# Performance work log

Hardware: AMD Instinct MI355X
Metric: run time of the kernel (lower is better)

Reference implementation:

```python
import jax, jax.numpy as jnp
import numpy as np

N_NODES = 100000
N_EDGES = 3200000
N_GRAPHS = 2000
F_IN, H, N_CLS = 14, 64, 2


def _glorot(key, shape):
    lim = float(np.sqrt(6.0 / (shape[0] + shape[1])))
    return jax.random.uniform(key, shape, jnp.float32, -lim, lim)


def setup_inputs() -> dict:
    key = jax.random.key(0)
    ks = jax.random.split(key, 16)
    x = jax.random.normal(ks[0], (N_NODES, F_IN), jnp.float32)
    edge_index = jax.random.randint(ks[1], (2, N_EDGES), 0, N_NODES, jnp.int64)
    batch = jnp.sort(jax.random.randint(ks[2], (N_NODES,), 0, N_GRAPHS, jnp.int64))
    return {
        "x": x,
        "W1l": _glorot(ks[3], (F_IN, H)), "W1r": _glorot(ks[4], (F_IN, H)), "b1": jnp.zeros((H,), jnp.float32),
        "W2l": _glorot(ks[5], (H, H)), "W2r": _glorot(ks[6], (H, H)), "b2": jnp.zeros((H,), jnp.float32),
        "W3l": _glorot(ks[7], (H, H)), "W3r": _glorot(ks[8], (H, H)), "b3": jnp.zeros((H,), jnp.float32),
        "W4l": _glorot(ks[9], (H, N_CLS)), "W4r": _glorot(ks[10], (H, N_CLS)), "b4": jnp.zeros((N_CLS,), jnp.float32),
        "edge_index": edge_index,
        "batch": batch,
    }


def _sage_conv(x, Wl, Wr, b, src, dst, inv_deg):
    # mean-aggregate neighbor features: messages flow src -> dst (PyG SAGEConv default)
    agg = jax.ops.segment_sum(x[src], dst, num_segments=N_NODES) * inv_deg
    return agg @ Wl + x @ Wr + b


def reference(x, W1l, W1r, b1, W2l, W2r, b2, W3l, W3r, b3, W4l, W4r, b4, edge_index, batch):
    src, dst = edge_index[0], edge_index[1]
    ones = jnp.ones((src.shape[0],), x.dtype)
    deg = jax.ops.segment_sum(ones, dst, num_segments=N_NODES)
    inv_deg = (1.0 / jnp.maximum(deg, 1.0))[:, None]  # [N,1], isolated nodes -> 0 agg

    h = jax.nn.relu(_sage_conv(x, W1l, W1r, b1, src, dst, inv_deg))
    h = jax.nn.relu(_sage_conv(h, W2l, W2r, b2, src, dst, inv_deg))
    h = jax.nn.relu(_sage_conv(h, W3l, W3r, b3, src, dst, inv_deg))
    h = _sage_conv(h, W4l, W4r, b4, src, dst, inv_deg)

    # global_mean_pool over graphs
    gsum = jax.ops.segment_sum(h, batch, num_segments=N_GRAPHS)
    gcnt = jax.ops.segment_sum(jnp.ones((h.shape[0],), h.dtype), batch, num_segments=N_GRAPHS)
    pooled = gsum / jnp.maximum(gcnt, 1.0)[:, None]
    return jax.nn.log_softmax(pooled, axis=-1)
```

## Files before the change

kernel.cpp:

```cpp
#include <hip/hip_runtime.h>

#define NN 100000
#define NE 3200000
#define NG 2000
#define FIN 14
#define HD 64
#define NC 2

#define NBUK 256
#define BNODES 391
#define P1E 4096
#define BUFCAP 13312

typedef unsigned int uint;

__device__ __forceinline__ uint pack2bf16(float a, float b) {
    uint ua = __float_as_uint(a), ub = __float_as_uint(b);
    ua = (ua + 0x7FFFu + ((ua >> 16) & 1u)) >> 16;
    ub = (ub + 0x7FFFu + ((ub >> 16) & 1u)) >> 16;
    return ua | (ub << 16);
}
__device__ __forceinline__ float bflo(uint u) { return __uint_as_float(u << 16); }
__device__ __forceinline__ float bfhi(uint u) { return __uint_as_float(u & 0xFFFF0000u); }


__global__ __launch_bounds__(256) void k_hist_bucket(const int* __restrict__ dst,
                                                     int* __restrict__ bkcnt) {
    __shared__ int cnt[NBUK];
    int t = threadIdx.x;
    cnt[t] = 0;
    __syncthreads();
    int e0 = blockIdx.x * P1E;
    int m = NE - e0; if (m > P1E) m = P1E;
    for (int e = t; e < m; e += 256) atomicAdd(&cnt[dst[e0 + e] / BNODES], 1);
    __syncthreads();
    if (cnt[t] > 0) atomicAdd(&bkcnt[t], cnt[t]);
}

__global__ void k_scanb(const int* __restrict__ bkcnt, int* __restrict__ bbase,
                        int* __restrict__ bcur) {
    __shared__ int tmp[NBUK];
    int t = threadIdx.x;
    int v = bkcnt[t];
    tmp[t] = v;
    __syncthreads();
    for (int off = 1; off < NBUK; off <<= 1) {
        int u = (t >= off) ? tmp[t - off] : 0;
        __syncthreads();
        tmp[t] += u;
        __syncthreads();
    }
    int excl = tmp[t] - v;
    bbase[t] = excl;
    bcur[t] = excl;
    if (t == NBUK - 1) bbase[NBUK] = tmp[t];
}

__global__ void k_gbounds(const int* __restrict__ batch, int* __restrict__ gstart,
                          int* __restrict__ gend) {
    int i = blockIdx.x * blockDim.x + threadIdx.x;
    if (i < NN) {
        int b = batch[i];
        if (i == 0 || batch[i - 1] != b) gstart[b] = i;
        if (i == NN - 1 || batch[i + 1] != b) gend[b] = i + 1;
    }
}

__global__ __launch_bounds__(256) void k_pass1(
    const int* __restrict__ src, const int* __restrict__ dst,
    int* __restrict__ bcur, int* __restrict__ pairs) {
    __shared__ int cnt[NBUK];
    __shared__ int scanb[NBUK + 1];
    __shared__ int cur[NBUK];
    __shared__ int gbase[NBUK];
    __shared__ int pbuf[P1E];
    __shared__ unsigned char bsl[P1E];
    int t = threadIdx.x;
    int e0 = blockIdx.x * P1E;
    int m = NE - e0; if (m > P1E) m = P1E;
    cnt[t] = 0;
    __syncthreads();
    int ds[16], ss[16], bk[16];
#pragma unroll
    for (int j = 0; j < 16; ++j) {
        int e = t + j * 256;
        if (e < m) {
            ds[j] = dst[e0 + e];
            ss[j] = src[e0 + e];
            bk[j] = ds[j] / BNODES;
            atomicAdd(&cnt[bk[j]], 1);
        } else bk[j] = -1;
    }
    __syncthreads();
    int v = cnt[t];
    scanb[t] = v;
    __syncthreads();
    for (int off = 1; off < 256; off <<= 1) {
        int u = (t >= off) ? scanb[t - off] : 0;
        __syncthreads();
        scanb[t] += u;
        __syncthreads();
    }
    int excl = scanb[t] - v;
    scanb[t] = excl;
    cur[t] = excl;
    if (t == 255) scanb[256] = excl + v;
    __syncthreads();
#pragma unroll
    for (int j = 0; j < 16; ++j) {
        if (bk[j] >= 0) {
            int p = atomicAdd(&cur[bk[j]], 1);
            pbuf[p] = ss[j] | ((ds[j] - bk[j] * BNODES) << 17);
            bsl[p] = (unsigned char)bk[j];
        }
    }
    int cb = scanb[t + 1] - scanb[t];
    if (cb > 0) gbase[t] = atomicAdd(&bcur[t], cb);
    __syncthreads();
    for (int s = t; s < m; s += 256) {
        int b = bsl[s];
        pairs[gbase[b] + (s - scanb[b])] = pbuf[s];
    }
}

__global__ __launch_bounds__(256) void k_pass2(
    const int* __restrict__ pairs, const int* __restrict__ bbase,
    int* __restrict__ deg, int* __restrict__ rs, int* __restrict__ csr) {
    __shared__ int buf1[BUFCAP];
    __shared__ int buf2[BUFCAP];
    __shared__ int cnt[512];
    __shared__ int rsl[512];
    __shared__ int cur[512];
    __shared__ int s1[256];
    int b = blockIdx.x;
    int n0 = b * BNODES;
    if (n0 >= NN) return;
    int nlocal = NN - n0; if (nlocal > BNODES) nlocal = BNODES;
    int t = threadIdx.x;
    int base = bbase[b];
    int m = bbase[b + 1] - base;
    bool fits = (m <= BUFCAP);
    cnt[t] = 0; cnt[t + 256] = 0;
    __syncthreads();
    for (int s = t; s < m; s += 256) {
        int pk = pairs[base + s];
        if (fits) buf1[s] = pk;
        atomicAdd(&cnt[(uint)pk >> 17], 1);
    }
    __syncthreads();
    int c0 = cnt[2 * t], c1 = cnt[2 * t + 1];
    int ps = c0 + c1;
    s1[t] = ps;
    __syncthreads();
    for (int off = 1; off < 256; off <<= 1) {
        int u = (t >= off) ? s1[t - off] : 0;
        __syncthreads();
        s1[t] += u;
        __syncthreads();
    }
    int pexcl = s1[t] - ps;
    rsl[2 * t] = pexcl;       cur[2 * t] = pexcl;
    rsl[2 * t + 1] = pexcl + c0; cur[2 * t + 1] = pexcl + c0;
    __syncthreads();
    for (int i = t; i < nlocal; i += 256) {
        deg[n0 + i] = cnt[i];
        rs[n0 + i] = base + rsl[i];
    }
    if (fits) {
        for (int s = t; s < m; s += 256) {
            int pk = buf1[s];
            int p = atomicAdd(&cur[(uint)pk >> 17], 1);
            buf2[p] = pk & 0x1FFFF;
        }
        __syncthreads();
        for (int s = t; s < m; s += 256) csr[base + s] = buf2[s];
    } else {
        for (int s = t; s < m; s += 256) {
            int pk = pairs[base + s];
            int p = atomicAdd(&cur[(uint)pk >> 17], 1);
            csr[base + p] = pk & 0x1FFFF;
        }
    }
}


__global__ void k_packx(const float* __restrict__ x, uint* __restrict__ xb) {
    int t = blockIdx.x * blockDim.x + threadIdx.x;
    if (t < NN * 8) {
        int row = t >> 3, q = t & 7;
        int j0 = 2 * q, j1 = 2 * q + 1;
        float f0 = (j0 < FIN) ? x[row * FIN + j0] : 0.f;
        float f1 = (j1 < FIN) ? x[row * FIN + j1] : 0.f;
        xb[t] = pack2bf16(f0, f1);
    }
}


__global__ __launch_bounds__(256, 6) void k_layer1(
    const float* __restrict__ x, const uint* __restrict__ xb, uint* __restrict__ hbout,
    const float* __restrict__ Wl, const float* __restrict__ Wr, const float* __restrict__ b,
    const int* __restrict__ rs, const int* __restrict__ deg, const int* __restrict__ csr) {
    __shared__ float2 sW[FIN][HD];
    __shared__ float sb[HD];
    __shared__ float2 sAH[4][16];
    for (int i = threadIdx.x; i < FIN * HD; i += 256) {
        int k = i >> 6, j = i & 63;
        sW[k][j] = make_float2(Wl[i], Wr[i]);
    }
    if (threadIdx.x < HD) sb[threadIdx.x] = b[threadIdx.x];
    __syncthreads();
    int lane = threadIdx.x & 63, wid = threadIdx.x >> 6;
    int sub = lane >> 3;
    int fq = lane & 7;
    int ngroups = (NN + 3) / 4;
    for (int g = blockIdx.x; g < ngroups; g += gridDim.x) {
        int n = g * 4 + wid;
        bool act = n < NN;
        if (act) {
            int s0 = rs[n], d = deg[n];
            float xv = (lane < FIN) ? x[n * FIN + lane] : 0.f;
            float2 a0 = make_float2(0.f, 0.f), a1 = a0, a2 = a0, a3 = a0;
            float2 a4 = a0, a5 = a0, a6 = a0, a7 = a0;
            for (int base = 0; base < d; base += 64) {
                int rem = d - base; if (rem > 64) rem = 64;
                int idxv = (lane < rem) ? csr[s0 + base + lane] : 0;
                int j = 0;
                for (; j + 64 <= rem; j += 64) {
                    int i0 = __shfl(idxv, j + 0 + sub);
                    int i1 = __shfl(idxv, j + 8 + sub);
                    int i2 = __shfl(idxv, j + 16 + sub);
                    int i3 = __shfl(idxv, j + 24 + sub);
                    int i4 = __shfl(idxv, j + 32 + sub);
                    int i5 = __shfl(idxv, j + 40 + sub);
                    int i6 = __shfl(idxv, j + 48 + sub);
                    int i7 = __shfl(idxv, j + 56 + sub);
                    uint u;
                    u = xb[(size_t)i0 * 8 + fq]; a0.x += bflo(u); a0.y += bfhi(u);
                    u = xb[(size_t)i1 * 8 + fq]; a1.x += bflo(u); a1.y += bfhi(u);
                    u = xb[(size_t)i2 * 8 + fq]; a2.x += bflo(u); a2.y += bfhi(u);
                    u = xb[(size_t)i3 * 8 + fq]; a3.x += bflo(u); a3.y += bfhi(u);
                    u = xb[(size_t)i4 * 8 + fq]; a4.x += bflo(u); a4.y += bfhi(u);
                    u = xb[(size_t)i5 * 8 + fq]; a5.x += bflo(u); a5.y += bfhi(u);
                    u = xb[(size_t)i6 * 8 + fq]; a6.x += bflo(u); a6.y += bfhi(u);
                    u = xb[(size_t)i7 * 8 + fq]; a7.x += bflo(u); a7.y += bfhi(u);
                }
                for (; j + 8 <= rem; j += 8) {
                    int i0 = __shfl(idxv, j + sub);
                    uint u = xb[(size_t)i0 * 8 + fq];
                    a0.x += bflo(u); a0.y += bfhi(u);
                }
                if (j < rem) {
                    int i0 = __shfl(idxv, j + sub);
                    if (sub < rem - j) {
                        uint u = xb[(size_t)i0 * 8 + fq];
                        a0.x += bflo(u); a0.y += bfhi(u);
                    }
                }
            }
            a0.x += a1.x + a2.x + a3.x + a4.x + a5.x + a6.x + a7.x;
            a0.y += a1.y + a2.y + a3.y + a4.y + a5.y + a6.y + a7.y;
            for (int off = 8; off <= 32; off <<= 1) {
                a0.x += __shfl_xor(a0.x, off);
                a0.y += __shfl_xor(a0.y, off);
            }
            float inv = 1.0f / (float)(d > 1 ? d : 1);
            float e0 = __shfl(a0.x, lane >> 1);
            float e1 = __shfl(a0.y, lane >> 1);
            float sel = (lane & 1) ? e1 : e0;
            if (lane < 16) sAH[wid][lane] = make_float2((lane < FIN) ? sel * inv : 0.f, xv);
        }
        float out = sb[lane];
#pragma unroll
        for (int k = 0; k < FIN; ++k) {
            float2 w = sW[k][lane];
            float2 ah = sAH[wid][k];
            out += ah.x * w.x + ah.y * w.y;
        }
        out = fmaxf(out, 0.f);
        float o2 = __shfl_xor(out, 1);
        if (act && !(lane & 1)) hbout[(size_t)n * 32 + (lane >> 1)] = pack2bf16(out, o2);
    }
}


__device__ __forceinline__ void bfadd4(float4& A, uint2 U) {
    A.x += bflo(U.x); A.y += bfhi(U.x);
    A.z += bflo(U.y); A.w += bfhi(U.y);
}

template <bool FUSEZ>
__global__ __launch_bounds__(256, 6) void k_layerH(
    const uint* __restrict__ hbin, uint* __restrict__ hbout,
    const float* __restrict__ Wl, const float* __restrict__ Wr, const float* __restrict__ b,
    const float* __restrict__ W4l, float* __restrict__ z,
    const int* __restrict__ rs, const int* __restrict__ deg, const int* __restrict__ csr) {
    __shared__ uint sWp[HD][HD];
    __shared__ float sb[HD], sW4l[HD * NC];
    __shared__ float2 sAH[4][HD];
    for (int i = threadIdx.x; i < HD * HD; i += 256) {
        int k = i >> 6, j = i & 63;
        sWp[k][j] = pack2bf16(Wl[i], Wr[i]);
    }
    if (threadIdx.x < HD) sb[threadIdx.x] = b[threadIdx.x];
    if (FUSEZ && threadIdx.x < HD * NC) sW4l[threadIdx.x] = W4l[threadIdx.x];
    __syncthreads();
    const uint2* hb2 = (const uint2*)hbin;
    int lane = threadIdx.x & 63, wid = threadIdx.x >> 6;
    int sub = lane >> 4;
    int fq = lane & 15;
    int ngroups = (NN + 3) / 4;
    for (int g = blockIdx.x; g < ngroups; g += gridDim.x) {
        int n = g * 4 + wid;
        bool act = n < NN;
        if (act) {
            int s0 = rs[n], d = deg[n];
            uint hu = hbin[(size_t)n * 32 + (lane >> 1)];
            float hv = (lane & 1) ? bfhi(hu) : bflo(hu);
            float4 A0 = make_float4(0.f, 0.f, 0.f, 0.f);
            float4 A1 = A0, A2 = A0, A3 = A0, A4 = A0, A5 = A0, A6 = A0, A7 = A0;
            for (int base = 0; base < d; base += 64) {
                int rem = d - base; if (rem > 64) rem = 64;
                int idxv = (lane < rem) ? csr[s0 + base + lane] : 0;
                int j = 0;
                for (; j + 32 <= rem; j += 32) {
                    int i0 = __shfl(idxv, j + 0 + sub);
                    int i1 = __shfl(idxv, j + 4 + sub);
                    int i2 = __shfl(idxv, j + 8 + sub);
                    int i3 = __shfl(idxv, j + 12 + sub);
                    int i4 = __shfl(idxv, j + 16 + sub);
                    int i5 = __shfl(idxv, j + 20 + sub);
                    int i6 = __shfl(idxv, j + 24 + sub);
                    int i7 = __shfl(idxv, j + 28 + sub);
                    bfadd4(A0, hb2[(size_t)i0 * 16 + fq]);
                    bfadd4(A1, hb2[(size_t)i1 * 16 + fq]);
                    bfadd4(A2, hb2[(size_t)i2 * 16 + fq]);
                    bfadd4(A3, hb2[(size_t)i3 * 16 + fq]);
                    bfadd4(A4, hb2[(size_t)i4 * 16 + fq]);
                    bfadd4(A5, hb2[(size_t)i5 * 16 + fq]);
                    bfadd4(A6, hb2[(size_t)i6 * 16 + fq]);
                    bfadd4(A7, hb2[(size_t)i7 * 16 + fq]);
                }
                for (; j + 4 <= rem; j += 4) {
                    int i0 = __shfl(idxv, j + sub);
                    bfadd4(A0, hb2[(size_t)i0 * 16 + fq]);
                }
                if (j < rem) {
                    int i0 = __shfl(idxv, j + sub);
                    if (sub < rem - j) bfadd4(A0, hb2[(size_t)i0 * 16 + fq]);
                }
            }
            A0.x += A1.x + A2.x + A3.x + A4.x + A5.x + A6.x + A7.x;
            A0.y += A1.y + A2.y + A3.y + A4.y + A5.y + A6.y + A7.y;
            A0.z += A1.z + A2.z + A3.z + A4.z + A5.z + A6.z + A7.z;
            A0.w += A1.w + A2.w + A3.w + A4.w + A5.w + A6.w + A7.w;
            for (int off = 16; off <= 32; off <<= 1) {
                A0.x += __shfl_xor(A0.x, off);
                A0.y += __shfl_xor(A0.y, off);
                A0.z += __shfl_xor(A0.z, off);
                A0.w += __shfl_xor(A0.w, off);
            }
            float inv = 1.0f / (float)(d > 1 ? d : 1);
            A0.x *= inv; A0.y *= inv; A0.z *= inv; A0.w *= inv;
            float e0 = __shfl(A0.x, lane >> 2);
            float e1 = __shfl(A0.y, lane >> 2);
            float e2 = __shfl(A0.z, lane >> 2);
            float e3 = __shfl(A0.w, lane >> 2);
            int c = lane & 3;
            float sel = (c == 0) ? e0 : (c == 1) ? e1 : (c == 2) ? e2 : e3;
            sAH[wid][lane] = make_float2(sel, hv);
        }
        float out = sb[lane];
#pragma unroll 8
        for (int k = 0; k < HD; ++k) {
            uint wu = sWp[k][lane];
            float2 ah = sAH[wid][k];
            out += ah.x * bflo(wu) + ah.y * bfhi(wu);
        }
        out = fmaxf(out, 0.f);
        float o2 = __shfl_xor(out, 1);
        if (act && !(lane & 1)) hbout[(size_t)n * 32 + (lane >> 1)] = pack2bf16(out, o2);
        if (FUSEZ) {
            float r0 = out * sW4l[lane * NC + 0];
            float r1 = out * sW4l[lane * NC + 1];
            for (int off = 32; off; off >>= 1) {
                r0 += __shfl_xor(r0, off);
                r1 += __shfl_xor(r1, off);
            }
            if (act && lane == 0) ((float2*)z)[n] = make_float2(r0, r1);
        }
    }
}


__global__ __launch_bounds__(256) void k_pool(
    const uint* __restrict__ h3, const float* __restrict__ z,
    const float* __restrict__ W4r, const float* __restrict__ b4,
    const int* __restrict__ rs, const int* __restrict__ deg, const int* __restrict__ csr,
    const int* __restrict__ batch, float* __restrict__ gsum) {
    __shared__ float sW[HD * NC];
    if (threadIdx.x < HD * NC) sW[threadIdx.x] = W4r[threadIdx.x];
    __syncthreads();
    const float2* z2 = (const float2*)z;
    int lane = threadIdx.x & 63, wid = threadIdx.x >> 6;
    int stride = gridDim.x * 4;
    for (int n = blockIdx.x * 4 + wid; n < NN; n += stride) {
        float r0 = 0.f, r1 = 0.f;
        if (lane < 32) {
            uint u = h3[(size_t)n * 32 + lane];
            float f0 = bflo(u), f1 = bfhi(u);
            r0 = f0 * sW[(2 * lane) * NC + 0] + f1 * sW[(2 * lane + 1) * NC + 0];
            r1 = f0 * sW[(2 * lane) * NC + 1] + f1 * sW[(2 * lane + 1) * NC + 1];
        }
        int s0 = rs[n], d = deg[n];
        float a0 = 0.f, a1 = 0.f;
        for (int j = lane; j < d; j += 64) {
            int s = csr[s0 + j];
            float2 zv = z2[s];
            a0 += zv.x;
            a1 += zv.y;
        }
        for (int off = 32; off; off >>= 1) {
            r0 += __shfl_xor(r0, off);
            r1 += __shfl_xor(r1, off);
            a0 += __shfl_xor(a0, off);
            a1 += __shfl_xor(a1, off);
        }
        if (lane == 0) {
            float inv = 1.0f / (float)(d > 1 ? d : 1);
            float o0 = a0 * inv + r0 + b4[0];
            float o1 = a1 * inv + r1 + b4[1];
            int gg = batch[n];
            atomicAdd(&gsum[gg * 2 + 0], o0);
            atomicAdd(&gsum[gg * 2 + 1], o1);
        }
    }
}

__global__ void k_final(const float* __restrict__ gsum, const int* __restrict__ gstart,
                        const int* __restrict__ gend, float* __restrict__ out) {
    int g = blockIdx.x * blockDim.x + threadIdx.x;
    if (g < NG) {
        int cnt = gend[g] - gstart[g];
        float inv = 1.0f / (float)(cnt > 1 ? cnt : 1);
        float p0 = gsum[g * 2 + 0] * inv;
        float p1 = gsum[g * 2 + 1] * inv;
        float m = fmaxf(p0, p1);
        float lse = m + logf(expf(p0 - m) + expf(p1 - m));
        out[g * 2 + 0] = p0 - lse;
        out[g * 2 + 1] = p1 - lse;
    }
}


extern "C" void kernel_launch(void* const* d_in, const int* in_sizes, int n_in,
                              void* d_out, int out_size, void* d_ws, size_t ws_size,
                              hipStream_t stream) {
    const float* x   = (const float*)d_in[0];
    const float* W1l = (const float*)d_in[1];
    const float* W1r = (const float*)d_in[2];
    const float* b1  = (const float*)d_in[3];
    const float* W2l = (const float*)d_in[4];
    const float* W2r = (const float*)d_in[5];
    const float* b2  = (const float*)d_in[6];
    const float* W3l = (const float*)d_in[7];
    const float* W3r = (const float*)d_in[8];
    const float* b3  = (const float*)d_in[9];
    const float* W4l = (const float*)d_in[10];
    const float* W4r = (const float*)d_in[11];
    const float* b4  = (const float*)d_in[12];
    const int* ei    = (const int*)d_in[13];
    const int* batch = (const int*)d_in[14];
    const int* src = ei;
    const int* dst = ei + NE;
    float* out = (float*)d_out;

    char* w = (char*)d_ws;
    int* deg    = (int*)w; w += (size_t)NN * 4;
    int* rs     = (int*)w; w += (size_t)NN * 4;
    int* csr    = (int*)w; w += (size_t)NE * 4;
    int* gstart = (int*)w; w += (size_t)NG * 4;
    int* gend   = (int*)w; w += (size_t)NG * 4;
    int* bkcnt  = (int*)w; w += NBUK * 4;
    int* bbase  = (int*)w; w += (NBUK + 1) * 4;
    int* bcur   = (int*)w; w += NBUK * 4;
    w = (char*)(((uintptr_t)w + 255) & ~(uintptr_t)255);
    uint* xb    = (uint*)w; w += (size_t)NN * 8 * 4;
    uint* hbA   = (uint*)w; w += (size_t)NN * 32 * 4;
    uint* hbB   = (uint*)w; w += (size_t)NN * 32 * 4;
    float* z    = (float*)w; w += (size_t)NN * NC * 4;
    float* gsum = (float*)w; w += (size_t)NG * NC * 4;
    int* pairs = (int*)hbB;

    const int P1B = (NE + P1E - 1) / P1E;

    hipMemsetAsync(bkcnt, 0, NBUK * 4, stream);
    hipMemsetAsync(gstart, 0, (size_t)NG * 4, stream);
    hipMemsetAsync(gend, 0, (size_t)NG * 4, stream);
    hipMemsetAsync(gsum, 0, (size_t)NG * NC * 4, stream);

    k_hist_bucket<<<P1B, 256, 0, stream>>>(dst, bkcnt);
    k_packx<<<(NN * 8 + 255) / 256, 256, 0, stream>>>(x, xb);
    k_gbounds<<<(NN + 255) / 256, 256, 0, stream>>>(batch, gstart, gend);
    k_scanb<<<1, NBUK, 0, stream>>>(bkcnt, bbase, bcur);
    k_pass1<<<P1B, 256, 0, stream>>>(src, dst, bcur, pairs);
    k_pass2<<<NBUK, 256, 0, stream>>>(pairs, bbase, deg, rs, csr);

    k_layer1<<<1536, 256, 0, stream>>>(x, xb, hbA, W1l, W1r, b1, rs, deg, csr);
    k_layerH<false><<<1536, 256, 0, stream>>>(hbA, hbB, W2l, W2r, b2, nullptr, nullptr, rs, deg, csr);
    k_layerH<true><<<1536, 256, 0, stream>>>(hbB, hbA, W3l, W3r, b3, W4l, z, rs, deg, csr);
    k_pool<<<2048, 256, 0, stream>>>(hbA, z, W4r, b4, rs, deg, csr, batch, gsum);
    k_final<<<(NG + 255) / 256, 256, 0, stream>>>(gsum, gstart, gend, out);
}
```

Before: 468.5 us.

## Tile hidden-layer gathers by source-node range so each pass stays cache-resident

The CSR build now sorts each destination's neighbors into eight source-node ranges and records per-range offsets in a new rs9 array. The hidden-layer kernels give each wave a fixed chunk of 25 destination nodes and sweep the source ranges in order. Per-node accumulators are kept in registers across sweeps, so that gathered feature rows come from a smaller, cache-resident slice of the feature table. In exchange there is more index metadata traffic, heavier register pressure (occupancy hint lowered from 6 to 4), less latency hiding in the gather (two loads per step instead of eight), and possible load imbalance from the fixed node chunks.

Measured after the change: 749.1 us. 1.6x slower.

```diff
diff --git a/kernel.cpp b/kernel.cpp
--- a/kernel.cpp
+++ b/kernel.cpp
@@ -11,6 +11,12 @@
 #define BNODES 391
 #define P1E 4096
 #define BUFCAP 13312
+
+#define NT 8
+#define TNODES 12500
+#define NCELL (BNODES * NT)
+#define NCELLP 3328
+#define NPW 25
 
 typedef unsigned int uint;
 
@@ -125,12 +131,12 @@
 
 __global__ __launch_bounds__(256) void k_pass2(
     const int* __restrict__ pairs, const int* __restrict__ bbase,
-    int* __restrict__ deg, int* __restrict__ rs, int* __restrict__ csr) {
-    __shared__ int buf1[BUFCAP];
+    int* __restrict__ deg, int* __restrict__ rs, int* __restrict__ rs9,
+    int* __restrict__ csr) {
     __shared__ int buf2[BUFCAP];
-    __shared__ int cnt[512];
-    __shared__ int rsl[512];
-    __shared__ int cur[512];
+    __shared__ int cnt[NCELLP];
+    __shared__ int off[NCELLP + 1];
+    __shared__ int cur[NCELLP];
     __shared__ int s1[256];
     int b = blockIdx.x;
     int n0 = b * BNODES;
@@ -139,46 +145,61 @@
     int t = threadIdx.x;
     int base = bbase[b];
     int m = bbase[b + 1] - base;
-    bool fits = (m <= BUFCAP);
-    cnt[t] = 0; cnt[t + 256] = 0;
+    for (int k = t; k < NCELLP; k += 256) cnt[k] = 0;
     __syncthreads();
     for (int s = t; s < m; s += 256) {
         int pk = pairs[base + s];
-        if (fits) buf1[s] = pk;
-        atomicAdd(&cnt[(uint)pk >> 17], 1);
-    }
-    __syncthreads();
-    int c0 = cnt[2 * t], c1 = cnt[2 * t + 1];
-    int ps = c0 + c1;
-    s1[t] = ps;
-    __syncthreads();
-    for (int off = 1; off < 256; off <<= 1) {
-        int u = (t >= off) ? s1[t - off] : 0;
+        int ln = (uint)pk >> 17;
+        int sr = pk & 0x1FFFF;
+        atomicAdd(&cnt[ln * NT + sr / TNODES], 1);
+    }
+    __syncthreads();
+    int loc[13];
+    int run = 0;
+#pragma unroll
+    for (int k = 0; k < 13; ++k) { loc[k] = run; run += cnt[t * 13 + k]; }
+    s1[t] = run;
+    __syncthreads();
+    for (int o = 1; o < 256; o <<= 1) {
+        int u = (t >= o) ? s1[t - o] : 0;
         __syncthreads();
         s1[t] += u;
         __syncthreads();
     }
-    int pexcl = s1[t] - ps;
-    rsl[2 * t] = pexcl;       cur[2 * t] = pexcl;
-    rsl[2 * t + 1] = pexcl + c0; cur[2 * t + 1] = pexcl + c0;
+    int excl = s1[t] - run;
+#pragma unroll
+    for (int k = 0; k < 13; ++k) {
+        int val = excl + loc[k];
+        off[t * 13 + k] = val;
+        cur[t * 13 + k] = val;
+    }
+    if (t == 0) off[NCELLP] = m;
     __syncthreads();
     for (int i = t; i < nlocal; i += 256) {
-        deg[n0 + i] = cnt[i];
-        rs[n0 + i] = base + rsl[i];
-    }
+        int o0 = off[i * NT];
+        int o8 = off[(i + 1) * NT];
+        deg[n0 + i] = o8 - o0;
+        rs[n0 + i] = base + o0;
+#pragma unroll
+        for (int st = 0; st < NT; ++st) rs9[(size_t)(n0 + i) * 9 + st] = base + off[i * NT + st];
+        rs9[(size_t)(n0 + i) * 9 + 8] = base + o8;
+    }
+    bool fits = (m <= BUFCAP);
     if (fits) {
         for (int s = t; s < m; s += 256) {
-            int pk = buf1[s];
-            int p = atomicAdd(&cur[(uint)pk >> 17], 1);
-            buf2[p] = pk & 0x1FFFF;
+            int pk = pairs[base + s];
+            int ln = (uint)pk >> 17, sr = pk & 0x1FFFF;
+            int p = atomicAdd(&cur[ln * NT + sr / TNODES], 1);
+            buf2[p] = sr;
         }
         __syncthreads();
         for (int s = t; s < m; s += 256) csr[base + s] = buf2[s];
     } else {
         for (int s = t; s < m; s += 256) {
             int pk = pairs[base + s];
-            int p = atomicAdd(&cur[(uint)pk >> 17], 1);
-            csr[base + p] = pk & 0x1FFFF;
+            int ln = (uint)pk >> 17, sr = pk & 0x1FFFF;
+            int p = atomicAdd(&cur[ln * NT + sr / TNODES], 1);
+            csr[base + p] = sr;
         }
     }
 }
@@ -283,19 +304,15 @@
 }
 
 
-__device__ __forceinline__ void bfadd4(float4& A, uint2 U) {
-    A.x += bflo(U.x); A.y += bfhi(U.x);
-    A.z += bflo(U.y); A.w += bfhi(U.y);
-}
-
 template <bool FUSEZ>
-__global__ __launch_bounds__(256, 6) void k_layerH(
+__global__ __launch_bounds__(256, 4) void k_layerH(
     const uint* __restrict__ hbin, uint* __restrict__ hbout,
     const float* __restrict__ Wl, const float* __restrict__ Wr, const float* __restrict__ b,
     const float* __restrict__ W4l, float* __restrict__ z,
-    const int* __restrict__ rs, const int* __restrict__ deg, const int* __restrict__ csr) {
+    const int* __restrict__ rs9, const int* __restrict__ csr) {
     __shared__ uint sWp[HD][HD];
     __shared__ float sb[HD], sW4l[HD * NC];
+    __shared__ uint sSp[4][NPW][32];
     __shared__ float2 sAH[4][HD];
     for (int i = threadIdx.x; i < HD * HD; i += 256) {
         int k = i >> 6, j = i & 63;
@@ -304,81 +321,67 @@
     if (threadIdx.x < HD) sb[threadIdx.x] = b[threadIdx.x];
     if (FUSEZ && threadIdx.x < HD * NC) sW4l[threadIdx.x] = W4l[threadIdx.x];
     __syncthreads();
-    const uint2* hb2 = (const uint2*)hbin;
-    int lane = threadIdx.x & 63, wid = threadIdx.x >> 6;
-    int sub = lane >> 4;
-    int fq = lane & 15;
-    int ngroups = (NN + 3) / 4;
-    for (int g = blockIdx.x; g < ngroups; g += gridDim.x) {
-        int n = g * 4 + wid;
-        bool act = n < NN;
-        if (act) {
-            int s0 = rs[n], d = deg[n];
-            uint hu = hbin[(size_t)n * 32 + (lane >> 1)];
-            float hv = (lane & 1) ? bfhi(hu) : bflo(hu);
-            float4 A0 = make_float4(0.f, 0.f, 0.f, 0.f);
-            float4 A1 = A0, A2 = A0, A3 = A0, A4 = A0, A5 = A0, A6 = A0, A7 = A0;
-            for (int base = 0; base < d; base += 64) {
-                int rem = d - base; if (rem > 64) rem = 64;
-                int idxv = (lane < rem) ? csr[s0 + base + lane] : 0;
-                int j = 0;
-                for (; j + 32 <= rem; j += 32) {
-                    int i0 = __shfl(idxv, j + 0 + sub);
-                    int i1 = __shfl(idxv, j + 4 + sub);
-                    int i2 = __shfl(idxv, j + 8 + sub);
-                    int i3 = __shfl(idxv, j + 12 + sub);
-                    int i4 = __shfl(idxv, j + 16 + sub);
-                    int i5 = __shfl(idxv, j + 20 + sub);
-                    int i6 = __shfl(idxv, j + 24 + sub);
-                    int i7 = __shfl(idxv, j + 28 + sub);
-                    bfadd4(A0, hb2[(size_t)i0 * 16 + fq]);
-                    bfadd4(A1, hb2[(size_t)i1 * 16 + fq]);
-                    bfadd4(A2, hb2[(size_t)i2 * 16 + fq]);
-                    bfadd4(A3, hb2[(size_t)i3 * 16 + fq]);
-                    bfadd4(A4, hb2[(size_t)i4 * 16 + fq]);
-                    bfadd4(A5, hb2[(size_t)i5 * 16 + fq]);
-                    bfadd4(A6, hb2[(size_t)i6 * 16 + fq]);
-                    bfadd4(A7, hb2[(size_t)i7 * 16 + fq]);
-                }
-                for (; j + 4 <= rem; j += 4) {
-                    int i0 = __shfl(idxv, j + sub);
-                    bfadd4(A0, hb2[(size_t)i0 * 16 + fq]);
-                }
-                if (j < rem) {
-                    int i0 = __shfl(idxv, j + sub);
-                    if (sub < rem - j) bfadd4(A0, hb2[(size_t)i0 * 16 + fq]);
+    int lane = threadIdx.x & 63;
+    int wid = __builtin_amdgcn_readfirstlane(threadIdx.x >> 6);
+    int sub = lane >> 5;
+    int q = lane & 31;
+    int n0 = (blockIdx.x * 4 + wid) * NPW;
+    float2 acc[NPW];
+#pragma unroll
+    for (int i = 0; i < NPW; ++i) acc[i] = make_float2(0.f, 0.f);
+    for (int st = 0; st < NT; ++st) {
+#pragma unroll
+        for (int i = 0; i < NPW; ++i) {
+            int n = n0 + i;
+            if (n < NN) {
+                int s0 = rs9[(size_t)n * 9 + st];
+                int e  = rs9[(size_t)n * 9 + st + 1];
+                int c = e - s0;
+                for (int bs = 0; bs < c; bs += 64) {
+                    int rem = c - bs; if (rem > 64) rem = 64;
+                    int idx = (lane < rem) ? csr[s0 + bs + lane] : 0;
+                    for (int j = 0; j < rem; j += 4) {
+                        int sA = __shfl(idx, j + sub);
+                        int sB = __shfl(idx, j + 2 + sub);
+                        uint uA = hbin[(uint)sA * 32u + q];
+                        uint uB = hbin[(uint)sB * 32u + q];
+                        if (j + sub < rem)     { acc[i].x += bflo(uA); acc[i].y += bfhi(uA); }
+                        if (j + 2 + sub < rem) { acc[i].x += bflo(uB); acc[i].y += bfhi(uB); }
+                    }
                 }
             }
-            A0.x += A1.x + A2.x + A3.x + A4.x + A5.x + A6.x + A7.x;
-            A0.y += A1.y + A2.y + A3.y + A4.y + A5.y + A6.y + A7.y;
-            A0.z += A1.z + A2.z + A3.z + A4.z + A5.z + A6.z + A7.z;
-            A0.w += A1.w + A2.w + A3.w + A4.w + A5.w + A6.w + A7.w;
-            for (int off = 16; off <= 32; off <<= 1) {
-                A0.x += __shfl_xor(A0.x, off);
-                A0.y += __shfl_xor(A0.y, off);
-                A0.z += __shfl_xor(A0.z, off);
-                A0.w += __shfl_xor(A0.w, off);
-            }
+        }
+    }
+#pragma unroll
+    for (int i = 0; i < NPW; ++i) {
+        int n = n0 + i;
+        float ax = acc[i].x + __shfl_xor(acc[i].x, 32);
+        float ay = acc[i].y + __shfl_xor(acc[i].y, 32);
+        if (n < NN) {
+            int d = rs9[(size_t)n * 9 + 8] - rs9[(size_t)n * 9];
             float inv = 1.0f / (float)(d > 1 ? d : 1);
-            A0.x *= inv; A0.y *= inv; A0.z *= inv; A0.w *= inv;
-            float e0 = __shfl(A0.x, lane >> 2);
-            float e1 = __shfl(A0.y, lane >> 2);
-            float e2 = __shfl(A0.z, lane >> 2);
-            float e3 = __shfl(A0.w, lane >> 2);
-            int c = lane & 3;
-            float sel = (c == 0) ? e0 : (c == 1) ? e1 : (c == 2) ? e2 : e3;
-            sAH[wid][lane] = make_float2(sel, hv);
-        }
-        float out = sb[lane];
+            if (lane < 32) sSp[wid][i][q] = pack2bf16(ax * inv, ay * inv);
+        }
+    }
+    for (int i = 0; i < NPW; ++i) {
+        int n = n0 + i;
+        if (n >= NN) break;
+        uint au = sSp[wid][i][lane >> 1];
+        float aggk = (lane & 1) ? bfhi(au) : bflo(au);
+        uint hu = hbin[(uint)n * 32u + (lane >> 1)];
+        float hv = (lane & 1) ? bfhi(hu) : bflo(hu);
+        sAH[wid][lane] = make_float2(aggk, hv);
+        float outA = sb[lane], outB = 0.f;
 #pragma unroll 8
         for (int k = 0; k < HD; ++k) {
             uint wu = sWp[k][lane];
             float2 ah = sAH[wid][k];
-            out += ah.x * bflo(wu) + ah.y * bfhi(wu);
-        }
-        out = fmaxf(out, 0.f);
+            outA += ah.x * bflo(wu);
+            outB += ah.y * bfhi(wu);
+        }
+        float out = fmaxf(outA + outB, 0.f);
         float o2 = __shfl_xor(out, 1);
-        if (act && !(lane & 1)) hbout[(size_t)n * 32 + (lane >> 1)] = pack2bf16(out, o2);
+        if (!(lane & 1)) hbout[(uint)n * 32u + (lane >> 1)] = pack2bf16(out, o2);
         if (FUSEZ) {
             float r0 = out * sW4l[lane * NC + 0];
             float r1 = out * sW4l[lane * NC + 1];
@@ -386,7 +389,7 @@
                 r0 += __shfl_xor(r0, off);
                 r1 += __shfl_xor(r1, off);
             }
-            if (act && lane == 0) ((float2*)z)[n] = make_float2(r0, r1);
+            if (lane == 0) ((float2*)z)[n] = make_float2(r0, r1);
         }
     }
 }
@@ -478,6 +481,7 @@
     int* deg    = (int*)w; w += (size_t)NN * 4;
     int* rs     = (int*)w; w += (size_t)NN * 4;
     int* csr    = (int*)w; w += (size_t)NE * 4;
+    int* rs9    = (int*)w; w += (size_t)NN * 9 * 4;
     int* gstart = (int*)w; w += (size_t)NG * 4;
     int* gend   = (int*)w; w += (size_t)NG * 4;
     int* bkcnt  = (int*)w; w += NBUK * 4;
@@ -503,11 +507,11 @@
     k_gbounds<<<(NN + 255) / 256, 256, 0, stream>>>(batch, gstart, gend);
     k_scanb<<<1, NBUK, 0, stream>>>(bkcnt, bbase, bcur);
     k_pass1<<<P1B, 256, 0, stream>>>(src, dst, bcur, pairs);
-    k_pass2<<<NBUK, 256, 0, stream>>>(pairs, bbase, deg, rs, csr);
+    k_pass2<<<NBUK, 256, 0, stream>>>(pairs, bbase, deg, rs, rs9, csr);
 
     k_layer1<<<1536, 256, 0, stream>>>(x, xb, hbA, W1l, W1r, b1, rs, deg, csr);
-    k_layerH<false><<<1536, 256, 0, stream>>>(hbA, hbB, W2l, W2r, b2, nullptr, nullptr, rs, deg, csr);
-    k_layerH<true><<<1536, 256, 0, stream>>>(hbB, hbA, W3l, W3r, b3, W4l, z, rs, deg, csr);
+    k_layerH<false><<<1000, 256, 0, stream>>>(hbA, hbB, W2l, W2r, b2, nullptr, nullptr, rs9, csr);
+    k_layerH<true><<<1000, 256, 0, stream>>>(hbB, hbA, W3l, W3r, b3, W4l, z, rs9, csr);
     k_pool<<<2048, 256, 0, stream>>>(hbA, z, W4r, b4, rs, deg, csr, batch, gsum);
     k_final<<<(NG + 255) / 256, 256, 0, stream>>>(gsum, gstart, gend, out);
 }
```
